# Optimization experiments

Measured on AMD Instinct MI355X. Metric: run time of the kernel, lower is better.

The kernel has to match this reference:

```python
import jax, jax.numpy as jnp
import numpy as np

N, K = 4096, 4096
TOKENS = 8192
GROUP_SIZE = 128
NBIT = 4


def setup_inputs() -> dict:
    key = jax.random.key(0)
    k1, k2, k3, k4, k5 = jax.random.split(key, 5)
    x = jax.random.normal(k1, (TOKENS, K), dtype=jnp.float32)
    weight_qvals = jax.random.randint(k2, (N, K), 0, 1 << NBIT, dtype=jnp.int32)
    n_groups = K // GROUP_SIZE
    weight_scales = jax.random.uniform(k3, (N, n_groups), dtype=jnp.float32, minval=0.005, maxval=0.02)
    weight_zeros = jax.random.normal(k4, (N, n_groups), dtype=jnp.float32) * 0.05
    bias = jax.random.normal(k5, (N,), dtype=jnp.float32)
    return {"x": x, "weight_qvals": weight_qvals, "weight_scales": weight_scales,
            "weight_zeros": weight_zeros, "bias": bias, "group_size": GROUP_SIZE}


def reference(x, weight_qvals, weight_scales, weight_zeros, bias, group_size):
    n, k = weight_qvals.shape
    n_groups = k // group_size
    # dequantize: w = q * scale + zeros   (zeros already holds -zero_point*scale)
    q = weight_qvals.astype(jnp.float32).reshape(n, n_groups, group_size)
    w = q * weight_scales[:, :, None] + weight_zeros[:, :, None]  # [n, n_groups, g]
    w = w.reshape(n, k)
    # linear: out[t, n] = sum_k x[t, k] * w[n, k]
    out = jnp.einsum('tk,nk->tn', x, w) + bias
    return out
```

## Files before the change

kernel.cpp:

```cpp
#include <hip/hip_runtime.h>

#define M_TOK 8192
#define N_OUT 4096
#define K_DIM 4096
#define NGROUPS 32
#define K_TILES 128

typedef __bf16 bf16x8 __attribute__((ext_vector_type(8)));
typedef __bf16 bf16x4 __attribute__((ext_vector_type(4)));
typedef float  f32x4  __attribute__((ext_vector_type(4)));

#define GLOBAL_CVP const __attribute__((address_space(1))) void*
#define LDS_VP __attribute__((address_space(3))) void*

#define XBLOCKS 2048
#define WBLOCKS 1024
__global__ __launch_bounds__(256)
void prep_kernel(const float* __restrict__ x, __bf16* __restrict__ xb,
                 const int* __restrict__ wq, const float* __restrict__ scales,
                 const float* __restrict__ zeros, __bf16* __restrict__ wb) {
    if (blockIdx.x < XBLOCKS) {
        const size_t total = (size_t)M_TOK * K_DIM / 8;
        for (size_t i = (size_t)blockIdx.x * blockDim.x + threadIdx.x; i < total;
             i += (size_t)XBLOCKS * blockDim.x) {
            const float4 v0 = ((const float4*)x)[2 * i];
            const float4 v1 = ((const float4*)x)[2 * i + 1];
            bf16x8 b;
            b[0] = (__bf16)v0.x; b[1] = (__bf16)v0.y; b[2] = (__bf16)v0.z; b[3] = (__bf16)v0.w;
            b[4] = (__bf16)v1.x; b[5] = (__bf16)v1.y; b[6] = (__bf16)v1.z; b[7] = (__bf16)v1.w;
            ((bf16x8*)xb)[i] = b;
        }
    } else {
        const size_t total = (size_t)N_OUT * K_DIM / 8;
        for (size_t i = (size_t)(blockIdx.x - XBLOCKS) * blockDim.x + threadIdx.x; i < total;
             i += (size_t)WBLOCKS * blockDim.x) {
            const int4 q0 = ((const int4*)wq)[2 * i];
            const int4 q1 = ((const int4*)wq)[2 * i + 1];
            const size_t e = i * 8;
            const int row = (int)(e >> 12);
            const int g   = ((int)e & 4095) >> 7;
            const float s = scales[row * NGROUPS + g];
            const float z = zeros [row * NGROUPS + g];
            bf16x8 b;
            b[0] = (__bf16)fmaf((float)q0.x, s, z);
            b[1] = (__bf16)fmaf((float)q0.y, s, z);
            b[2] = (__bf16)fmaf((float)q0.z, s, z);
            b[3] = (__bf16)fmaf((float)q0.w, s, z);
            b[4] = (__bf16)fmaf((float)q1.x, s, z);
            b[5] = (__bf16)fmaf((float)q1.y, s, z);
            b[6] = (__bf16)fmaf((float)q1.z, s, z);
            b[7] = (__bf16)fmaf((float)q1.w, s, z);
            ((bf16x8*)wb)[i] = b;
        }
    }
}

__global__ __launch_bounds__(512, 2)
void gemm_bt256_kernel(const __bf16* __restrict__ A, const __bf16* __restrict__ B,
                       const float* __restrict__ bias, float* __restrict__ out) {
    __shared__ __bf16 As[4 * 8192];
    __shared__ __bf16 Bs[4 * 8192];

    const int tid  = threadIdx.x;
    const int wid  = tid >> 6;
    const int lane = tid & 63;

    const int s   = blockIdx.x;
    const int swz = (s & 7) * 64 + (s >> 3);
    const int m0  = (swz & 31) * 256;
    const int n0  = (swz >> 5) * 256;

    const int lrow  = lane & 15;
    const int quad  = lane >> 4;
    const int wmRow = (wid >> 2) * 128;
    const int wnRow = (wid & 3) * 64;
    const int sq = (quad ^ ((lrow >> 1) & 3)) * 8;

    const int scol = ((lane & 3) ^ ((lane >> 3) & 3)) * 8;
    const __bf16* Abase = A + (size_t)(m0 + wid * 16 + (lane >> 2)) * K_DIM + scol;
    const __bf16* Bbase = B + (size_t)(n0 + wid * 16 + (lane >> 2)) * K_DIM + scol;

    f32x4 acc[8][4];
#pragma unroll
    for (int i = 0; i < 8; ++i)
#pragma unroll
        for (int j = 0; j < 4; ++j)
            acc[i][j] = (f32x4){0.f, 0.f, 0.f, 0.f};

#define STAGE(T)                                                                            \
    {                                                                                       \
        const int    _s  = (T) & 3;                                                         \
        const size_t _k  = (size_t)(T) * 32;                                                \
        const __bf16* _ga = Abase + _k;                                                     \
        const __bf16* _gb = Bbase + _k;                                                     \
        __bf16* _la = (__bf16*)As + _s * 8192 + wid * 512;                                  \
        __bf16* _lb = (__bf16*)Bs + _s * 8192 + wid * 512;                                  \
        __builtin_amdgcn_global_load_lds((GLOBAL_CVP)(_ga), (LDS_VP)(_la), 16, 0, 0);       \
        __builtin_amdgcn_global_load_lds((GLOBAL_CVP)(_ga + (size_t)128 * K_DIM),           \
                                         (LDS_VP)(_la + 4096), 16, 0, 0);                   \
        __builtin_amdgcn_global_load_lds((GLOBAL_CVP)(_gb), (LDS_VP)(_lb), 16, 0, 0);       \
        __builtin_amdgcn_global_load_lds((GLOBAL_CVP)(_gb + (size_t)128 * K_DIM),           \
                                         (LDS_VP)(_lb + 4096), 16, 0, 0);                   \
    }

#define KBODY(T)                                                                            \
    {                                                                                       \
        const int _s = (T) & 3;                                                             \
        const __bf16* _As = (const __bf16*)As + _s * 8192;                                  \
        const __bf16* _Bs = (const __bf16*)Bs + _s * 8192;                                  \
        bf16x8 _af[8], _bf[4];                                                              \
        _Pragma("unroll")                                                                   \
        for (int _j = 0; _j < 4; ++_j)                                                      \
            _bf[_j] = *(const bf16x8*)&_Bs[(wnRow + _j * 16 + lrow) * 32 + sq];             \
        _Pragma("unroll")                                                                   \
        for (int _i = 0; _i < 8; ++_i)                                                      \
            _af[_i] = *(const bf16x8*)&_As[(wmRow + _i * 16 + lrow) * 32 + sq];             \
        __builtin_amdgcn_s_setprio(1);                                                      \
        _Pragma("unroll")                                                                   \
        for (int _i = 0; _i < 8; ++_i)                                                      \
            _Pragma("unroll")                                                               \
            for (int _j = 0; _j < 4; ++_j)                                                  \
                acc[_i][_j] = __builtin_amdgcn_mfma_f32_16x16x32_bf16(_af[_i], _bf[_j],     \
                                                                      acc[_i][_j], 0, 0, 0);\
        __builtin_amdgcn_s_setprio(0);                                                      \
    }

#define SYNC(VM)                                                                            \
    {                                                                                       \
        __builtin_amdgcn_sched_barrier(0);                                                  \
        asm volatile("s_waitcnt vmcnt(" #VM ")" ::: "memory");                              \
        __builtin_amdgcn_s_barrier();                                                       \
        __builtin_amdgcn_sched_barrier(0);                                                  \
    }

    STAGE(0); STAGE(1); STAGE(2);
    SYNC(8);

#pragma unroll 4
    for (int t = 0; t < K_TILES - 3; ++t) {
        STAGE(t + 3);
        KBODY(t);
        SYNC(8);
    }
    KBODY(K_TILES - 3); SYNC(4);
    KBODY(K_TILES - 2); SYNC(0);
    KBODY(K_TILES - 1);

#undef STAGE
#undef KBODY
#undef SYNC

#pragma unroll
    for (int j = 0; j < 4; ++j) {
        const int col = n0 + wnRow + j * 16 + lrow;
        const float bv = bias[col];
#pragma unroll
        for (int i = 0; i < 8; ++i) {
            const int rowb = m0 + wmRow + i * 16 + quad * 4;
#pragma unroll
            for (int r = 0; r < 4; ++r)
                out[(size_t)(rowb + r) * N_OUT + col] = acc[i][j][r] + bv;
        }
    }
}

#define LDS_STRIDE 40
__global__ __launch_bounds__(256)
void qlinear_fused_kernel(const float* __restrict__ x,
                          const int*   __restrict__ wq,
                          const float* __restrict__ scales,
                          const float* __restrict__ zeros,
                          const float* __restrict__ bias,
                          float*       __restrict__ out)
{
    __shared__ __bf16 As[128 * LDS_STRIDE];
    __shared__ __bf16 Bs[128 * LDS_STRIDE];
    const int tid  = threadIdx.x;
    const int m0   = blockIdx.x * 128;
    const int n0   = blockIdx.y * 128;
    const int wave = tid >> 6;
    const int lane = tid & 63;
    const int wm   = (wave & 1) * 64;
    const int wn   = (wave >> 1) * 64;
    const int lrow = lane & 15;
    const int quad = lane >> 4;
    const int srow = tid >> 3;
    const int scol = (tid & 7) * 4;

    f32x4 acc[4][4];
#pragma unroll
    for (int i = 0; i < 4; i++)
#pragma unroll
        for (int j = 0; j < 4; j++)
            acc[i][j] = (f32x4){0.f, 0.f, 0.f, 0.f};

    for (int k0 = 0; k0 < K_DIM; k0 += 32) {
        const int g = k0 >> 7;
#pragma unroll
        for (int rr = 0; rr < 4; rr++) {
            const int row = srow + rr * 32;
            const float4 v = *(const float4*)(x + (size_t)(m0 + row) * K_DIM + k0 + scol);
            bf16x4 b;
            b[0] = (__bf16)v.x; b[1] = (__bf16)v.y;
            b[2] = (__bf16)v.z; b[3] = (__bf16)v.w;
            *(bf16x4*)&As[row * LDS_STRIDE + scol] = b;
        }
#pragma unroll
        for (int rr = 0; rr < 4; rr++) {
            const int row = srow + rr * 32;
            const int4 q = *(const int4*)(wq + (size_t)(n0 + row) * K_DIM + k0 + scol);
            const float s = scales[(n0 + row) * NGROUPS + g];
            const float z = zeros [(n0 + row) * NGROUPS + g];
            bf16x4 b;
            b[0] = (__bf16)fmaf((float)q.x, s, z);
            b[1] = (__bf16)fmaf((float)q.y, s, z);
            b[2] = (__bf16)fmaf((float)q.z, s, z);
            b[3] = (__bf16)fmaf((float)q.w, s, z);
            *(bf16x4*)&Bs[row * LDS_STRIDE + scol] = b;
        }
        __syncthreads();
        bf16x8 af[4], bfr[4];
#pragma unroll
        for (int i = 0; i < 4; i++) {
            af[i]  = *(const bf16x8*)&As[(wm + i * 16 + lrow) * LDS_STRIDE + quad * 8];
            bfr[i] = *(const bf16x8*)&Bs[(wn + i * 16 + lrow) * LDS_STRIDE + quad * 8];
        }
#pragma unroll
        for (int i = 0; i < 4; i++)
#pragma unroll
            for (int j = 0; j < 4; j++)
                acc[i][j] = __builtin_amdgcn_mfma_f32_16x16x32_bf16(af[i], bfr[j], acc[i][j], 0, 0, 0);
        __syncthreads();
    }
#pragma unroll
    for (int j = 0; j < 4; j++) {
        const int col = n0 + wn + j * 16 + lrow;
        const float bv = bias[col];
#pragma unroll
        for (int i = 0; i < 4; i++) {
            const int rowb = m0 + wm + i * 16 + quad * 4;
#pragma unroll
            for (int r = 0; r < 4; r++)
                out[(size_t)(rowb + r) * N_OUT + col] = acc[i][j][r] + bv;
        }
    }
}

extern "C" void kernel_launch(void* const* d_in, const int* in_sizes, int n_in,
                              void* d_out, int out_size, void* d_ws, size_t ws_size,
                              hipStream_t stream) {
    const float* x      = (const float*)d_in[0];
    const int*   wq     = (const int*)  d_in[1];
    const float* scales = (const float*)d_in[2];
    const float* zeros  = (const float*)d_in[3];
    const float* bias   = (const float*)d_in[4];
    float*       out    = (float*)d_out;

    const size_t xb_bytes = (size_t)M_TOK * K_DIM * 2;
    const size_t wb_bytes = (size_t)N_OUT * K_DIM * 2;

    if (ws_size >= xb_bytes + wb_bytes) {
        __bf16* xb = (__bf16*)d_ws;
        __bf16* wb = (__bf16*)((char*)d_ws + xb_bytes);
        prep_kernel<<<XBLOCKS + WBLOCKS, 256, 0, stream>>>(x, xb, wq, scales, zeros, wb);
        dim3 grid((M_TOK / 256) * (N_OUT / 256));
        gemm_bt256_kernel<<<grid, 512, 0, stream>>>(xb, wb, bias, out);
    } else {
        dim3 grid(M_TOK / 128, N_OUT / 128);
        qlinear_fused_kernel<<<grid, 256, 0, stream>>>(x, wq, scales, zeros, bias, out);
    }
}
```

Before: 529.8 us.

## Double-buffer MFMA fragments in registers to overlap LDS reads with MFMAs

The GEMM main loop now keeps two register sets of A/B fragments. It reads tile t+1 from LDS into one set while MFMAs run on the other, and the loop is manually unrolled by two with an explicit epilogue. The goal is to hide LDS read latency behind matrix-core work. In exchange it adds about 48 live VGPRs per thread. The wait tightens from vmcnt(8) to vmcnt(4), which shrinks how far global-to-LDS loads can run ahead.

New measurement: 575.9 us. 8.7% more time.

```diff
diff --git a/kernel.cpp b/kernel.cpp
--- a/kernel.cpp
+++ b/kernel.cpp
@@ -87,6 +87,8 @@
         for (int j = 0; j < 4; ++j)
             acc[i][j] = (f32x4){0.f, 0.f, 0.f, 0.f};
 
+    bf16x8 afA[8], bfA[4], afB[8], bfB[4];
+
 #define STAGE(T)                                                                            \
     {                                                                                       \
         const int    _s  = (T) & 3;                                                         \
@@ -103,24 +105,27 @@
                                          (LDS_VP)(_lb + 4096), 16, 0, 0);                   \
     }
 
-#define KBODY(T)                                                                            \
+#define FRAGS(AF, BF, T)                                                                    \
     {                                                                                       \
         const int _s = (T) & 3;                                                             \
         const __bf16* _As = (const __bf16*)As + _s * 8192;                                  \
         const __bf16* _Bs = (const __bf16*)Bs + _s * 8192;                                  \
-        bf16x8 _af[8], _bf[4];                                                              \
         _Pragma("unroll")                                                                   \
         for (int _j = 0; _j < 4; ++_j)                                                      \
-            _bf[_j] = *(const bf16x8*)&_Bs[(wnRow + _j * 16 + lrow) * 32 + sq];             \
+            BF[_j] = *(const bf16x8*)&_Bs[(wnRow + _j * 16 + lrow) * 32 + sq];              \
         _Pragma("unroll")                                                                   \
         for (int _i = 0; _i < 8; ++_i)                                                      \
-            _af[_i] = *(const bf16x8*)&_As[(wmRow + _i * 16 + lrow) * 32 + sq];             \
+            AF[_i] = *(const bf16x8*)&_As[(wmRow + _i * 16 + lrow) * 32 + sq];              \
+    }
+
+#define MFMAS(AF, BF)                                                                       \
+    {                                                                                       \
         __builtin_amdgcn_s_setprio(1);                                                      \
         _Pragma("unroll")                                                                   \
         for (int _i = 0; _i < 8; ++_i)                                                      \
             _Pragma("unroll")                                                               \
             for (int _j = 0; _j < 4; ++_j)                                                  \
-                acc[_i][_j] = __builtin_amdgcn_mfma_f32_16x16x32_bf16(_af[_i], _bf[_j],     \
+                acc[_i][_j] = __builtin_amdgcn_mfma_f32_16x16x32_bf16(AF[_i], BF[_j],       \
                                                                       acc[_i][_j], 0, 0, 0);\
         __builtin_amdgcn_s_setprio(0);                                                      \
     }
@@ -134,20 +139,29 @@
     }
 
     STAGE(0); STAGE(1); STAGE(2);
-    SYNC(8);
-
-#pragma unroll 4
-    for (int t = 0; t < K_TILES - 3; ++t) {
+    SYNC(4);
+    FRAGS(afA, bfA, 0);
+
+    for (int t = 0; t < K_TILES - 6; t += 2) {
         STAGE(t + 3);
-        KBODY(t);
-        SYNC(8);
-    }
-    KBODY(K_TILES - 3); SYNC(4);
-    KBODY(K_TILES - 2); SYNC(0);
-    KBODY(K_TILES - 1);
+        FRAGS(afB, bfB, t + 1);
+        MFMAS(afA, bfA);
+        SYNC(4);
+        STAGE(t + 4);
+        FRAGS(afA, bfA, t + 2);
+        MFMAS(afB, bfB);
+        SYNC(4);
+    }
+    STAGE(125); FRAGS(afB, bfB, 123); MFMAS(afA, bfA); SYNC(4);
+    STAGE(126); FRAGS(afA, bfA, 124); MFMAS(afB, bfB); SYNC(4);
+    STAGE(127); FRAGS(afB, bfB, 125); MFMAS(afA, bfA); SYNC(4);
+    FRAGS(afA, bfA, 126); MFMAS(afB, bfB); SYNC(0);
+    FRAGS(afB, bfB, 127); MFMAS(afA, bfA);
+    MFMAS(afB, bfB);
 
 #undef STAGE
-#undef KBODY
+#undef FRAGS
+#undef MFMAS
 #undef SYNC
 
 #pragma unroll
```

## Restructure bf16 GEMM main loop into 64-wide K tiles with ping-pong phases

Applied to the files above, without the earlier changes.

Moves the bf16 GEMM from four-stage 32-wide K tiles to double-buffered 64-wide K tiles with an 8-way XOR swizzle. Each K iteration is split into four MFMA sub-phases, each separated by barriers, and global-to-LDS loads for the A and B tiles are staggered across those phases in a ping-pong style schedule. The aim is better overlap of LDS reads, global loads and MFMA work and fewer loop iterations. In exchange it adds many more barriers per iteration and relies on careful waitcnt bookkeeping, so a miscount could cause hazards.

Result: slower. 569.4 us (+7.5%).

```diff
diff --git a/kernel.cpp b/kernel.cpp
--- a/kernel.cpp
+++ b/kernel.cpp
@@ -4,7 +4,7 @@
 #define N_OUT 4096
 #define K_DIM 4096
 #define NGROUPS 32
-#define K_TILES 128
+#define KT64 64
 
 typedef __bf16 bf16x8 __attribute__((ext_vector_type(8)));
 typedef __bf16 bf16x4 __attribute__((ext_vector_type(4)));
@@ -58,8 +58,8 @@
 __global__ __launch_bounds__(512, 2)
 void gemm_bt256_kernel(const __bf16* __restrict__ A, const __bf16* __restrict__ B,
                        const float* __restrict__ bias, float* __restrict__ out) {
-    __shared__ __bf16 As[4 * 8192];
-    __shared__ __bf16 Bs[4 * 8192];
+    __shared__ __bf16 As[32768];
+    __shared__ __bf16 Bs[32768];
 
     const int tid  = threadIdx.x;
     const int wid  = tid >> 6;
@@ -74,11 +74,19 @@
     const int quad  = lane >> 4;
     const int wmRow = (wid >> 2) * 128;
     const int wnRow = (wid & 3) * 64;
-    const int sq = (quad ^ ((lrow >> 1) & 3)) * 8;
-
-    const int scol = ((lane & 3) ^ ((lane >> 3) & 3)) * 8;
-    const __bf16* Abase = A + (size_t)(m0 + wid * 16 + (lane >> 2)) * K_DIM + scol;
-    const __bf16* Bbase = B + (size_t)(n0 + wid * 16 + (lane >> 2)) * K_DIM + scol;
+
+    const int g0 = ((quad)     ^ (lrow & 7)) * 8;
+    const int g1 = ((quad + 4) ^ (lrow & 7)) * 8;
+
+    const int srow = lane >> 3;
+    const int scol = ((lane & 7) ^ srow) * 8;
+    const __bf16* Asrc = A + (size_t)(m0 + wid * 16 + srow) * K_DIM + scol;
+    const __bf16* Bsrc = B + (size_t)(n0 + wid * 16 + srow) * K_DIM + scol;
+    const int ldst = wid * 1024 + lane * 8;
+
+    const __bf16* AhB = As + (wid >> 2) * 8192;
+    const __bf16* BhB = Bs + ((wid & 3) >> 1) * 8192;
+    const int lbB = ((wid & 3) & 1) * 64;
 
     f32x4 acc[8][4];
 #pragma unroll
@@ -87,68 +95,103 @@
         for (int j = 0; j < 4; ++j)
             acc[i][j] = (f32x4){0.f, 0.f, 0.f, 0.f};
 
-#define STAGE(T)                                                                            \
-    {                                                                                       \
-        const int    _s  = (T) & 3;                                                         \
-        const size_t _k  = (size_t)(T) * 32;                                                \
-        const __bf16* _ga = Abase + _k;                                                     \
-        const __bf16* _gb = Bbase + _k;                                                     \
-        __bf16* _la = (__bf16*)As + _s * 8192 + wid * 512;                                  \
-        __bf16* _lb = (__bf16*)Bs + _s * 8192 + wid * 512;                                  \
-        __builtin_amdgcn_global_load_lds((GLOBAL_CVP)(_ga), (LDS_VP)(_la), 16, 0, 0);       \
-        __builtin_amdgcn_global_load_lds((GLOBAL_CVP)(_ga + (size_t)128 * K_DIM),           \
-                                         (LDS_VP)(_la + 4096), 16, 0, 0);                   \
-        __builtin_amdgcn_global_load_lds((GLOBAL_CVP)(_gb), (LDS_VP)(_lb), 16, 0, 0);       \
-        __builtin_amdgcn_global_load_lds((GLOBAL_CVP)(_gb + (size_t)128 * K_DIM),           \
-                                         (LDS_VP)(_lb + 4096), 16, 0, 0);                   \
-    }
-
-#define KBODY(T)                                                                            \
-    {                                                                                       \
-        const int _s = (T) & 3;                                                             \
-        const __bf16* _As = (const __bf16*)As + _s * 8192;                                  \
-        const __bf16* _Bs = (const __bf16*)Bs + _s * 8192;                                  \
-        bf16x8 _af[8], _bf[4];                                                              \
-        _Pragma("unroll")                                                                   \
-        for (int _j = 0; _j < 4; ++_j)                                                      \
-            _bf[_j] = *(const bf16x8*)&_Bs[(wnRow + _j * 16 + lrow) * 32 + sq];             \
-        _Pragma("unroll")                                                                   \
-        for (int _i = 0; _i < 8; ++_i)                                                      \
-            _af[_i] = *(const bf16x8*)&_As[(wmRow + _i * 16 + lrow) * 32 + sq];             \
-        __builtin_amdgcn_s_setprio(1);                                                      \
-        _Pragma("unroll")                                                                   \
-        for (int _i = 0; _i < 8; ++_i)                                                      \
-            _Pragma("unroll")                                                               \
-            for (int _j = 0; _j < 4; ++_j)                                                  \
-                acc[_i][_j] = __builtin_amdgcn_mfma_f32_16x16x32_bf16(_af[_i], _bf[_j],     \
-                                                                      acc[_i][_j], 0, 0, 0);\
-        __builtin_amdgcn_s_setprio(0);                                                      \
-    }
-
-#define SYNC(VM)                                                                            \
-    {                                                                                       \
-        __builtin_amdgcn_sched_barrier(0);                                                  \
-        asm volatile("s_waitcnt vmcnt(" #VM ")" ::: "memory");                              \
+    bf16x8 af[8], bfA[4], bfB[4];
+
+#define SGA(TT, H)                                                                          \
+    {                                                                                       \
+        __bf16* _d = (__bf16*)As + ((TT) & 1) * 16384 + (H) * 8192 + ldst;                  \
+        const __bf16* _g = Asrc + (size_t)((H) * 128) * K_DIM + (size_t)(TT) * 64;          \
+        __builtin_amdgcn_global_load_lds((GLOBAL_CVP)_g, (LDS_VP)_d, 16, 0, 0);             \
+        __builtin_amdgcn_global_load_lds((GLOBAL_CVP)(_g + (size_t)8 * K_DIM),              \
+                                         (LDS_VP)(_d + 512), 16, 0, 0);                     \
+    }
+#define SGB(TT, H)                                                                          \
+    {                                                                                       \
+        __bf16* _d = (__bf16*)Bs + ((TT) & 1) * 16384 + (H) * 8192 + ldst;                  \
+        const __bf16* _g = Bsrc + (size_t)((H) * 128) * K_DIM + (size_t)(TT) * 64;          \
+        __builtin_amdgcn_global_load_lds((GLOBAL_CVP)_g, (LDS_VP)_d, 16, 0, 0);             \
+        __builtin_amdgcn_global_load_lds((GLOBAL_CVP)(_g + (size_t)8 * K_DIM),              \
+                                         (LDS_VP)(_d + 512), 16, 0, 0);                     \
+    }
+#define RDA(MH)                                                                             \
+    _Pragma("unroll") for (int _i = 0; _i < 4; ++_i) {                                      \
+        af[_i]     = *(const bf16x8*)&Ab[((MH) * 64 + _i * 16 + lrow) * 64 + g0];           \
+        af[4 + _i] = *(const bf16x8*)&Ab[((MH) * 64 + _i * 16 + lrow) * 64 + g1];           \
+    }
+#define RDB(NH, BF)                                                                         \
+    _Pragma("unroll") for (int _j = 0; _j < 2; ++_j) {                                      \
+        BF[_j]     = *(const bf16x8*)&Bb[(lbB + (NH) * 32 + _j * 16 + lrow) * 64 + g0];     \
+        BF[2 + _j] = *(const bf16x8*)&Bb[(lbB + (NH) * 32 + _j * 16 + lrow) * 64 + g1];     \
+    }
+#define MF16(MH, NH, BF)                                                                    \
+    __builtin_amdgcn_s_setprio(1);                                                          \
+    _Pragma("unroll") for (int _i = 0; _i < 4; ++_i)                                        \
+    _Pragma("unroll") for (int _j = 0; _j < 2; ++_j) {                                      \
+        acc[(MH)*4+_i][(NH)*2+_j] = __builtin_amdgcn_mfma_f32_16x16x32_bf16(                \
+            af[_i], BF[_j], acc[(MH)*4+_i][(NH)*2+_j], 0, 0, 0);                            \
+        acc[(MH)*4+_i][(NH)*2+_j] = __builtin_amdgcn_mfma_f32_16x16x32_bf16(                \
+            af[4+_i], BF[2+_j], acc[(MH)*4+_i][(NH)*2+_j], 0, 0, 0);                        \
+    }                                                                                       \
+    __builtin_amdgcn_s_setprio(0);
+#define BAR                                                                                 \
+    {                                                                                       \
+        __builtin_amdgcn_sched_barrier(0);                                                  \
         __builtin_amdgcn_s_barrier();                                                       \
         __builtin_amdgcn_sched_barrier(0);                                                  \
     }
-
-    STAGE(0); STAGE(1); STAGE(2);
-    SYNC(8);
-
-#pragma unroll 4
-    for (int t = 0; t < K_TILES - 3; ++t) {
-        STAGE(t + 3);
-        KBODY(t);
-        SYNC(8);
-    }
-    KBODY(K_TILES - 3); SYNC(4);
-    KBODY(K_TILES - 2); SYNC(0);
-    KBODY(K_TILES - 1);
-
-#undef STAGE
-#undef KBODY
-#undef SYNC
+#define BARLG                                                                               \
+    {                                                                                       \
+        __builtin_amdgcn_sched_barrier(0);                                                  \
+        __builtin_amdgcn_s_barrier();                                                       \
+        asm volatile("s_waitcnt lgkmcnt(0)" ::: "memory");                                  \
+        __builtin_amdgcn_sched_barrier(0);                                                  \
+    }
+#define KITER(T, SA, SB, VMQ)                                                               \
+    {                                                                                       \
+        const int _b = (T) & 1;                                                             \
+        const __bf16* Ab = AhB + _b * 16384;                                                \
+        const __bf16* Bb = BhB + _b * 16384;                                                \
+                                                                                    \
+        RDA(0); RDB(0, bfA);                                                                \
+        if (SA) SGA((T) + 1, 0);                                                            \
+        asm volatile("s_waitcnt lgkmcnt(8)" ::: "memory");                                  \
+        BARLG; MF16(0, 0, bfA); BAR;                                                        \
+                                                                                    \
+        RDB(1, bfB);                                                                        \
+        if (SA) SGA((T) + 1, 1);                                                            \
+        BARLG; MF16(0, 1, bfB); BAR;                                                        \
+                                                                                    \
+        RDA(1);                                                                             \
+        if (SB) SGB((T) + 2, 0);                                                            \
+        BARLG; MF16(1, 1, bfB); BAR;                                                        \
+                                          \
+        if (SB) SGB((T) + 2, 1);                                                            \
+        BAR; MF16(1, 0, bfA);                                                               \
+        __builtin_amdgcn_sched_barrier(0);                                                  \
+        asm volatile("s_waitcnt vmcnt(" #VMQ ")" ::: "memory");                             \
+        __builtin_amdgcn_s_barrier();                                                       \
+        __builtin_amdgcn_sched_barrier(0);                                                  \
+    }
+
+    SGA(0, 0); SGA(0, 1); SGB(0, 0); SGB(0, 1); SGB(1, 0); SGB(1, 1);
+    asm volatile("s_waitcnt vmcnt(4)" ::: "memory");
+    __builtin_amdgcn_s_barrier();
+
+#pragma unroll 1
+    for (int t = 0; t < KT64 - 2; ++t) {
+        KITER(t, 1, 1, 4);
+    }
+    KITER(KT64 - 2, 1, 0, 0);
+    KITER(KT64 - 1, 0, 0, 0);
+
+#undef SGA
+#undef SGB
+#undef RDA
+#undef RDB
+#undef MF16
+#undef BAR
+#undef BARLG
+#undef KITER
 
 #pragma unroll
     for (int j = 0; j < 4; ++j) {
```
